# Kernel tuning notes

Hardware: AMD Instinct MI355X
Metric: run time of the kernel (lower is better)

The kernel has to match this reference:

```python
import jax, jax.numpy as jnp
import numpy as np

B, N, C, H, T = 64, 4096, 768, 12, 10


def setup_inputs() -> dict:
    key = jax.random.key(0)
    kx, kq, kk, kv, kp = jax.random.split(key, 5)
    std = 0.02  # trunc_normal std from _init_weights
    return {
        "x": jax.random.normal(kx, (B, N, C), jnp.float32),
        "Wq": std * jax.random.normal(kq, (C, C), jnp.float32),
        "Wk": std * jax.random.normal(kk, (C, C), jnp.float32),
        "Wv": std * jax.random.normal(kv, (C, C), jnp.float32),
        "Wp": std * jax.random.normal(kp, (C, C), jnp.float32),
        "bp": jnp.zeros((C,), jnp.float32),
        "nb_task_tokens": T,
    }


def reference(x, Wq, Wk, Wv, Wp, bp, nb_task_tokens):
    Bq, Nq, Cq = x.shape
    d = Cq // H
    scale = d ** -0.5
    Tt = nb_task_tokens
    # q only from the first T (task) tokens; k, v from all N tokens
    q = (x[:, :Tt] @ Wq).reshape(Bq, Tt, H, d).transpose(0, 2, 1, 3) * scale  # [B,H,T,d]
    k = (x @ Wk).reshape(Bq, Nq, H, d).transpose(0, 2, 1, 3)                  # [B,H,N,d]
    v = (x @ Wv).reshape(Bq, Nq, H, d).transpose(0, 2, 1, 3)                  # [B,H,N,d]
    attn = jnp.einsum("bhtd,bhnd->bhtn", q, k)                                # [B,H,T,N]
    # mask: task token i may attend to itself and to all patch tokens (cols >= T),
    # but not to other task tokens
    rows = jnp.arange(Tt)[:, None]
    cols = jnp.arange(Nq)[None, :]
    allowed = (cols >= Tt) | (cols == rows)                                   # [T,N]
    attn = jnp.where(allowed, attn, -jnp.inf)
    attn = jax.nn.softmax(attn, axis=-1)
    x_cls = jnp.einsum("bhtn,bhnd->bhtd", attn, v)                            # [B,H,T,d]
    x_cls = x_cls.transpose(0, 2, 1, 3).reshape(Bq, Tt, Cq)
    x_cls = x_cls @ Wp + bp
    return (x_cls, attn, v)
```

## Files before the change

### kernel.cpp

```cpp
#include <hip/hip_runtime.h>

typedef __attribute__((ext_vector_type(8))) short short8;
typedef __attribute__((ext_vector_type(4))) short short4v;
typedef __attribute__((ext_vector_type(4))) float f32x4;

__device__ __forceinline__ unsigned short f2bf(float f) {
  union { float f; unsigned u; } v; v.f = f;
  unsigned r = v.u + 0x7FFFu + ((v.u >> 16) & 1u);
  return (unsigned short)(r >> 16);
}

__device__ __forceinline__ void gload16(const void* g, void* l) {
  __builtin_amdgcn_global_load_lds(
      (const __attribute__((address_space(1))) void*)g,
      (__attribute__((address_space(3))) void*)l, 16, 0, 0);
}

__global__ __launch_bounds__(256) void conv_x(const float* __restrict__ x,
                                              unsigned short* __restrict__ xb) {
  const long total = 25165824;
  long stride = (long)gridDim.x * 256;
  for (long u = blockIdx.x * 256 + threadIdx.x; u < total; u += stride) {
    const float* p = x + u * 8;
    float4 a = *(const float4*)p;
    float4 b = *(const float4*)(p + 4);
    short8 h;
    h[0] = (short)f2bf(a.x); h[1] = (short)f2bf(a.y);
    h[2] = (short)f2bf(a.z); h[3] = (short)f2bf(a.w);
    h[4] = (short)f2bf(b.x); h[5] = (short)f2bf(b.y);
    h[6] = (short)f2bf(b.z); h[7] = (short)f2bf(b.w);
    *(short8*)(xb + u * 8) = h;
  }
}

__global__ __launch_bounds__(256) void prep_w(const float* __restrict__ Wk,
                                              const float* __restrict__ Wv,
                                              unsigned short* __restrict__ Wt) {
  int idx = blockIdx.x * 256 + threadIdx.x;
  int n = idx / 768, k = idx - n * 768;
  float w = (n < 768) ? Wk[k * 768 + n] : Wv[k * 768 + (n - 768)];
  Wt[idx] = f2bf(w);
}

__global__ __launch_bounds__(256) void q_proj(const float* __restrict__ x,
                                              const float* __restrict__ Wq,
                                              unsigned short* __restrict__ q_ws) {
  int b = blockIdx.x, tid = threadIdx.x;
  __shared__ float xr[7680];
  const float* xp = x + (long)b * 4096 * 768;
  for (int i = tid; i < 7680; i += 256) xr[i] = xp[i];
  for (int i = tid; i < 12 * 6 * 64; i += 256) {
    int h = i / 384, rem = i - h * 384;
    int t = 10 + rem / 64, d = rem & 63;
    q_ws[(((long)(b * 12 + h) * 16 + t) << 6) + d] = 0;
  }
  __syncthreads();
  float acc[10][3];
#pragma unroll
  for (int t = 0; t < 10; ++t) { acc[t][0] = 0.f; acc[t][1] = 0.f; acc[t][2] = 0.f; }
  for (int k = 0; k < 768; ++k) {
    const float* wr = Wq + (long)k * 768;
    float w0 = wr[tid], w1 = wr[tid + 256], w2 = wr[tid + 512];
#pragma unroll
    for (int t = 0; t < 10; ++t) {
      float xv = xr[t * 768 + k];
      acc[t][0] += xv * w0; acc[t][1] += xv * w1; acc[t][2] += xv * w2;
    }
  }
#pragma unroll
  for (int t = 0; t < 10; ++t) {
#pragma unroll
    for (int j = 0; j < 3; ++j) {
      int c = tid + j * 256;
      int h = c >> 6, d = c & 63;
      q_ws[(((long)(b * 12 + h) * 16 + t) << 6) + d] = f2bf(acc[t][j] * 0.125f);
    }
  }
}

__global__ __launch_bounds__(512, 2) void gemm_kv8(const unsigned short* __restrict__ xb,
                                                   const unsigned short* __restrict__ Wt,
                                                   unsigned short* __restrict__ k_ws,
                                                   float* __restrict__ v_out) {
  __shared__ char smem[131072];
#define A0T ((unsigned short*)(smem))
#define B0T ((unsigned short*)(smem + 32768))
#define A1T ((unsigned short*)(smem + 65536))
#define B1T ((unsigned short*)(smem + 98304))

  int bid = blockIdx.x;
  int lb = (bid & 7) * 768 + (bid >> 3);
  int mt = lb / 6, nt = lb - mt * 6;
  long m0 = (long)mt * 256; int n0 = nt * 256;
  int tid = threadIdx.x, lane = tid & 63;
  int uw = __builtin_amdgcn_readfirstlane(tid >> 6);
  int wm = uw >> 2, wn = uw & 3;
  int r16 = lane & 15, gk = lane >> 4;

  const unsigned short* xs = xb + m0 * 768;
  const unsigned short* wp = Wt + (long)n0 * 768;

  int srow8 = lane >> 3;
  int sch = ((lane & 7) ^ (srow8 & 7)) << 3;
  const unsigned short* sA = xs + (long)(uw * 8 + srow8) * 768 + sch;
  const unsigned short* sB = wp + (long)(uw * 8 + srow8) * 768 + sch;

  int ck0 = ((gk ^ (r16 & 7)) << 3);
  int ck1 = (((4 + gk) ^ (r16 & 7)) << 3);
  int arb = (wm * 128 + r16) * 64;
  int brb = (wn * 64 + r16) * 64;

  f32x4 acc[8][4];
#pragma unroll
  for (int i = 0; i < 8; ++i)
#pragma unroll
    for (int j = 0; j < 4; ++j) acc[i][j] = (f32x4){0.f, 0.f, 0.f, 0.f};

#define SGA(AT, I, KO) gload16(sA + (long)(I) * 49152 + (KO), (AT) + ((I) * 64 + uw * 8) * 64)
#define SGB(BT, I, KO) gload16(sB + (long)(I) * 49152 + (KO), (BT) + ((I) * 64 + uw * 8) * 64)
#define WBND asm volatile("s_waitcnt vmcnt(0)\n\ts_barrier" ::: "memory")
#define PBAR __builtin_amdgcn_s_barrier()

#define BODY(AC, BC, AN, BN, KOS, DOST)                                         \
  {                                                                             \
    short8 fa[4][2], fb0[2][2], fb1[2][2];                                      \
                    \
    if (DOST) { SGA(AN, 0, KOS); SGA(AN, 1, KOS); SGB(BN, 0, KOS); SGB(BN, 1, KOS); } \
    _Pragma("unroll")                                                           \
    for (int mi = 0; mi < 4; ++mi) {                                            \
      fa[mi][0] = *(const short8*)&AC[arb + mi * 1024 + ck0];                   \
      fa[mi][1] = *(const short8*)&AC[arb + mi * 1024 + ck1];                   \
    }                                                                           \
    _Pragma("unroll")                                                           \
    for (int ni = 0; ni < 2; ++ni) {                                            \
      fb0[ni][0] = *(const short8*)&BC[brb + ni * 1024 + ck0];                  \
      fb0[ni][1] = *(const short8*)&BC[brb + ni * 1024 + ck1];                  \
    }                                                                           \
    PBAR;                                                                       \
    __builtin_amdgcn_s_setprio(1);                                              \
    _Pragma("unroll")                                                           \
    for (int mi = 0; mi < 4; ++mi)                                              \
      _Pragma("unroll")                                                         \
      for (int ni = 0; ni < 2; ++ni) {                                          \
        acc[mi][ni] = __builtin_amdgcn_mfma_f32_16x16x32_bf16(fa[mi][0], fb0[ni][0], acc[mi][ni], 0, 0, 0); \
        acc[mi][ni] = __builtin_amdgcn_mfma_f32_16x16x32_bf16(fa[mi][1], fb0[ni][1], acc[mi][ni], 0, 0, 0); \
      }                                                                         \
    __builtin_amdgcn_s_setprio(0);                                              \
    PBAR;                                                                       \
                           \
    if (DOST) { SGA(AN, 2, KOS); SGA(AN, 3, KOS); SGB(BN, 2, KOS); SGB(BN, 3, KOS); } \
    _Pragma("unroll")                                                           \
    for (int ni = 0; ni < 2; ++ni) {                                            \
      fb1[ni][0] = *(const short8*)&BC[brb + (ni + 2) * 1024 + ck0];            \
      fb1[ni][1] = *(const short8*)&BC[brb + (ni + 2) * 1024 + ck1];            \
    }                                                                           \
    PBAR;                                                                       \
    __builtin_amdgcn_s_setprio(1);                                              \
    _Pragma("unroll")                                                           \
    for (int mi = 0; mi < 4; ++mi)                                              \
      _Pragma("unroll")                                                         \
      for (int ni = 0; ni < 2; ++ni) {                                          \
        acc[mi][ni + 2] = __builtin_amdgcn_mfma_f32_16x16x32_bf16(fa[mi][0], fb1[ni][0], acc[mi][ni + 2], 0, 0, 0); \
        acc[mi][ni + 2] = __builtin_amdgcn_mfma_f32_16x16x32_bf16(fa[mi][1], fb1[ni][1], acc[mi][ni + 2], 0, 0, 0); \
      }                                                                         \
    __builtin_amdgcn_s_setprio(0);                                              \
    PBAR;                                                                       \
                                       \
    _Pragma("unroll")                                                           \
    for (int mi = 0; mi < 4; ++mi) {                                            \
      fa[mi][0] = *(const short8*)&AC[arb + (mi + 4) * 1024 + ck0];             \
      fa[mi][1] = *(const short8*)&AC[arb + (mi + 4) * 1024 + ck1];             \
    }                                                                           \
    PBAR;                                                                       \
    __builtin_amdgcn_s_setprio(1);                                              \
    _Pragma("unroll")                                                           \
    for (int mi = 0; mi < 4; ++mi)                                              \
      _Pragma("unroll")                                                         \
      for (int ni = 0; ni < 2; ++ni) {                                          \
        acc[mi + 4][ni + 2] = __builtin_amdgcn_mfma_f32_16x16x32_bf16(fa[mi][0], fb1[ni][0], acc[mi + 4][ni + 2], 0, 0, 0); \
        acc[mi + 4][ni + 2] = __builtin_amdgcn_mfma_f32_16x16x32_bf16(fa[mi][1], fb1[ni][1], acc[mi + 4][ni + 2], 0, 0, 0); \
      }                                                                         \
    __builtin_amdgcn_s_setprio(0);                                              \
    PBAR;                                                                       \
                                 \
    __builtin_amdgcn_s_setprio(1);                                              \
    _Pragma("unroll")                                                           \
    for (int mi = 0; mi < 4; ++mi)                                              \
      _Pragma("unroll")                                                         \
      for (int ni = 0; ni < 2; ++ni) {                                          \
        acc[mi + 4][ni] = __builtin_amdgcn_mfma_f32_16x16x32_bf16(fa[mi][0], fb0[ni][0], acc[mi + 4][ni], 0, 0, 0); \
        acc[mi + 4][ni] = __builtin_amdgcn_mfma_f32_16x16x32_bf16(fa[mi][1], fb0[ni][1], acc[mi + 4][ni], 0, 0, 0); \
      }                                                                         \
    __builtin_amdgcn_s_setprio(0);                                              \
  }

  SGA(A0T, 0, 0); SGA(A0T, 1, 0); SGA(A0T, 2, 0); SGA(A0T, 3, 0);
  SGB(B0T, 0, 0); SGB(B0T, 1, 0); SGB(B0T, 2, 0); SGB(B0T, 3, 0);
  WBND;

#pragma unroll 1
  for (int t = 0; t < 12; t += 2) {
    BODY(A0T, B0T, A1T, B1T, (t + 1) * 64, true);
    WBND;
    BODY(A1T, B1T, A0T, B0T, (t + 2) * 64, (t + 2) < 12);
    WBND;
  }
#undef BODY
#undef SGA
#undef SGB
#undef WBND
#undef PBAR

  float* scr = (float*)smem + uw * 1088;
  bool is_k = (n0 < 768);
  int h = (is_k ? (n0 >> 6) : ((n0 - 768) >> 6)) + wn;
  int bq = (int)(m0 >> 12);
  int nb = (int)(m0 & 4095) + wm * 128;

#pragma unroll
  for (int mi = 0; mi < 8; ++mi) {
#pragma unroll
    for (int ni = 0; ni < 4; ++ni)
#pragma unroll
      for (int r = 0; r < 4; ++r)
        scr[(gk * 4 + r) * 68 + ni * 16 + r16] = acc[mi][ni][r];
    int nbase = nb + mi * 16;
    if (is_k) {
#pragma unroll
      for (int p = 0; p < 2; ++p) {
        int row = p * 8 + (lane >> 3), d0 = (lane & 7) << 3;
        float4 aa = *(const float4*)&scr[row * 68 + d0];
        float4 bb = *(const float4*)&scr[row * 68 + d0 + 4];
        short8 hh;
        hh[0] = (short)f2bf(aa.x); hh[1] = (short)f2bf(aa.y);
        hh[2] = (short)f2bf(aa.z); hh[3] = (short)f2bf(aa.w);
        hh[4] = (short)f2bf(bb.x); hh[5] = (short)f2bf(bb.y);
        hh[6] = (short)f2bf(bb.z); hh[7] = (short)f2bf(bb.w);
        *(short8*)&k_ws[((long)(bq * 12 + h) * 4096 + nbase + row) * 64 + d0] = hh;
      }
    } else {
#pragma unroll
      for (int p = 0; p < 4; ++p) {
        int row = p * 4 + (lane >> 4), d0 = (lane & 15) << 2;
        float4 aa = *(const float4*)&scr[row * 68 + d0];
        *(float4*)&v_out[((long)(bq * 12 + h) * 4096 + nbase + row) * 64 + d0] = aa;
      }
    }
  }
#undef A0T
#undef B0T
#undef A1T
#undef B1T
}

__global__ __launch_bounds__(256) void gemm_kv(const float* __restrict__ x,
                                               const unsigned short* __restrict__ Wt,
                                               unsigned short* __restrict__ k_ws,
                                               float* __restrict__ v_out) {
  __shared__ char lds[32768];
  int bid = blockIdx.x;
  int lb = (bid & 7) * 3072 + (bid >> 3);
  int mt = lb / 12, nt = lb - mt * 12;
  long m0 = (long)mt * 128; int n0 = nt * 128;
  int tid = threadIdx.x, lane = tid & 63;
  int wid = tid >> 6, wm = wid >> 1, wn = wid & 1;
  int rlo = lane & 15, gk = lane >> 4;

  const float* xs = x + m0 * 768;
  const unsigned short* wp = Wt + (long)n0 * 768;

  int arow0 = tid >> 3, ak4 = (tid & 7) << 2;
  int bn = tid >> 1, bg = (tid & 1) << 1;

  f32x4 acc[4][4];
#pragma unroll
  for (int i = 0; i < 4; ++i)
#pragma unroll
    for (int j = 0; j < 4; ++j) acc[i][j] = (f32x4){0.f, 0.f, 0.f, 0.f};

  float4 fA[4]; short8 wB[2];
#pragma unroll
  for (int it = 0; it < 4; ++it) {
    int row = it * 32 + arow0;
    fA[it] = *(const float4*)(xs + (long)row * 768 + ak4);
  }
#pragma unroll
  for (int i = 0; i < 2; ++i)
    wB[i] = *(const short8*)(wp + (long)bn * 768 + (bg + i) * 8);
#pragma unroll
  for (int it = 0; it < 4; ++it) {
    int row = it * 32 + arow0;
    short4v h;
    h[0] = (short)f2bf(fA[it].x); h[1] = (short)f2bf(fA[it].y);
    h[2] = (short)f2bf(fA[it].z); h[3] = (short)f2bf(fA[it].w);
    *(short4v*)(lds + row * 64 + ((ak4 * 2) ^ (((row >> 1) & 3) << 4))) = h;
  }
#pragma unroll
  for (int i = 0; i < 2; ++i)
    *(short8*)(lds + 16384 + bn * 64 + (((bg + i) * 16) ^ (((bn >> 1) & 3) << 4))) = wB[i];
  __syncthreads();

#pragma unroll 2
  for (int ks = 0; ks < 24; ++ks) {
    char* Ab = lds + (ks & 1) * 8192;
    char* Bb = lds + 16384 + (ks & 1) * 8192;
    bool pf = (ks + 1 < 24);
    if (pf) {
#pragma unroll
      for (int it = 0; it < 4; ++it) {
        int row = it * 32 + arow0;
        fA[it] = *(const float4*)(xs + (long)row * 768 + (ks + 1) * 32 + ak4);
      }
#pragma unroll
      for (int i = 0; i < 2; ++i)
        wB[i] = *(const short8*)(wp + (long)bn * 768 + (ks + 1) * 32 + (bg + i) * 8);
    }
    short8 af[4], bfr[4];
#pragma unroll
    for (int mi = 0; mi < 4; ++mi) {
      int row = wm * 64 + mi * 16 + rlo;
      af[mi] = *(const short8*)(Ab + row * 64 + ((gk * 16) ^ (((row >> 1) & 3) << 4)));
    }
#pragma unroll
    for (int ni = 0; ni < 4; ++ni) {
      int n = wn * 64 + ni * 16 + rlo;
      bfr[ni] = *(const short8*)(Bb + n * 64 + ((gk * 16) ^ (((n >> 1) & 3) << 4)));
    }
#pragma unroll
    for (int mi = 0; mi < 4; ++mi)
#pragma unroll
      for (int ni = 0; ni < 4; ++ni)
        acc[mi][ni] = __builtin_amdgcn_mfma_f32_16x16x32_bf16(af[mi], bfr[ni], acc[mi][ni], 0, 0, 0);
    if (pf) {
      char* An = lds + ((ks + 1) & 1) * 8192;
      char* Bn = lds + 16384 + ((ks + 1) & 1) * 8192;
#pragma unroll
      for (int it = 0; it < 4; ++it) {
        int row = it * 32 + arow0;
        short4v h;
        h[0] = (short)f2bf(fA[it].x); h[1] = (short)f2bf(fA[it].y);
        h[2] = (short)f2bf(fA[it].z); h[3] = (short)f2bf(fA[it].w);
        *(short4v*)(An + row * 64 + ((ak4 * 2) ^ (((row >> 1) & 3) << 4))) = h;
      }
#pragma unroll
      for (int i = 0; i < 2; ++i)
        *(short8*)(Bn + bn * 64 + (((bg + i) * 16) ^ (((bn >> 1) & 3) << 4))) = wB[i];
    }
    __syncthreads();
  }

  bool is_k = (n0 < 768);
  int cb = is_k ? n0 : n0 - 768;
#pragma unroll
  for (int ni = 0; ni < 4; ++ni) {
    int cc = cb + wn * 64 + ni * 16 + rlo;
    int h = cc >> 6, d = cc & 63;
#pragma unroll
    for (int mi = 0; mi < 4; ++mi) {
#pragma unroll
      for (int r = 0; r < 4; ++r) {
        long m = m0 + wm * 64 + mi * 16 + gk * 4 + r;
        int b = (int)(m >> 12), n = (int)(m & 4095);
        long off = ((long)(b * 12 + h) * 4096 + n) * 64 + d;
        float val = acc[mi][ni][r];
        if (is_k) k_ws[off] = f2bf(val);
        else      v_out[off] = val;
      }
    }
  }
}

__global__ __launch_bounds__(512) void attn_fused(const unsigned short* __restrict__ k_ws,
                                                  const unsigned short* __restrict__ q_ws,
                                                  const float* __restrict__ v_glob,
                                                  float* __restrict__ attn_out,
                                                  float* __restrict__ preproj) {
  __shared__ float red[8][16];
  __shared__ float rowmax[16];
  __shared__ float rowinv[16];
  __shared__ float scratch[8 * 256];

  int tid = threadIdx.x, lane = tid & 63, w = tid >> 6;
  int bh = blockIdx.x;
  int r16 = lane & 15, gk = lane >> 4;
  int trc = (r16 < 10) ? r16 : 9;

  const unsigned short* kp = k_ws + (long)bh * (4096 * 64);
  const unsigned short* qp = q_ws + (long)bh * 1024;
  float* sraw = attn_out + (long)bh * 40960;
  const float* vp = v_glob + (long)bh * (4096 * 64);

  short8 qf0 = *(const short8*)(qp + r16 * 64 + gk * 8);
  short8 qf1 = *(const short8*)(qp + r16 * 64 + 32 + gk * 8);

  float pmax = -3.0e38f;
  for (int ch = 0; ch < 32; ++ch) {
    int n0 = (w * 32 + ch) << 4;
    short8 kf0 = *(const short8*)(kp + (long)(n0 + r16) * 64 + gk * 8);
    short8 kf1 = *(const short8*)(kp + (long)(n0 + r16) * 64 + 32 + gk * 8);
    f32x4 d4 = (f32x4){0.f, 0.f, 0.f, 0.f};
    d4 = __builtin_amdgcn_mfma_f32_16x16x32_bf16(kf0, qf0, d4, 0, 0, 0);
    d4 = __builtin_amdgcn_mfma_f32_16x16x32_bf16(kf1, qf1, d4, 0, 0, 0);
    float sv[4];
#pragma unroll
    for (int r = 0; r < 4; ++r) {
      int n = n0 + gk * 4 + r;
      float s = d4[r];
      if (n < 10 && n != r16) s = -1e30f;
      sv[r] = s;
      pmax = fmaxf(pmax, s);
    }
    if (r16 < 10)
      *(float4*)(sraw + r16 * 4096 + n0 + gk * 4) = make_float4(sv[0], sv[1], sv[2], sv[3]);
  }
  pmax = fmaxf(pmax, __shfl_xor(pmax, 16));
  pmax = fmaxf(pmax, __shfl_xor(pmax, 32));
  if (lane < 16) red[w][lane] = pmax;
  __syncthreads();
  if (tid < 16) {
    float m = red[0][tid];
#pragma unroll
    for (int i = 1; i < 8; ++i) m = fmaxf(m, red[i][tid]);
    rowmax[tid] = m;
  }
  __syncthreads();

  float mx = rowmax[trc];
  float psum = 0.f;
  for (int ch = 0; ch < 16; ++ch) {
    int n0 = ((w * 16 + ch) << 5) + gk * 8;
    float4 a = *(const float4*)(sraw + trc * 4096 + n0);
    float4 b2 = *(const float4*)(sraw + trc * 4096 + n0 + 4);
    psum += __expf(a.x - mx) + __expf(a.y - mx) + __expf(a.z - mx) + __expf(a.w - mx)
          + __expf(b2.x - mx) + __expf(b2.y - mx) + __expf(b2.z - mx) + __expf(b2.w - mx);
  }
  psum += __shfl_xor(psum, 16);
  psum += __shfl_xor(psum, 32);
  if (lane < 16) red[w][lane] = psum;
  __syncthreads();
  if (tid < 16) {
    float s = 0.f;
#pragma unroll
    for (int i = 0; i < 8; ++i) s += red[i][tid];
    rowinv[tid] = 1.0f / s;
  }
  __syncthreads();

  int dc = w & 3, half = w >> 2;
  int d0 = dc << 4;
  float inv = rowinv[trc];
  f32x4 acc = (f32x4){0.f, 0.f, 0.f, 0.f};
  for (int kk = 0; kk < 64; ++kk) {
    int nr = half * 2048 + kk * 32 + gk * 8;
    float* sp = sraw + trc * 4096 + nr;
    float4 s0 = *(const float4*)(sp);
    float4 s1 = *(const float4*)(sp + 4);
    float p0 = __expf(s0.x - mx) * inv, p1 = __expf(s0.y - mx) * inv;
    float p2 = __expf(s0.z - mx) * inv, p3 = __expf(s0.w - mx) * inv;
    float p4 = __expf(s1.x - mx) * inv, p5 = __expf(s1.y - mx) * inv;
    float p6 = __expf(s1.z - mx) * inv, p7 = __expf(s1.w - mx) * inv;
    if (r16 < 10) {
      *(float4*)(sp)     = make_float4(p0, p1, p2, p3);
      *(float4*)(sp + 4) = make_float4(p4, p5, p6, p7);
    }
    short8 pa;
    pa[0] = (short)f2bf(p0); pa[1] = (short)f2bf(p1);
    pa[2] = (short)f2bf(p2); pa[3] = (short)f2bf(p3);
    pa[4] = (short)f2bf(p4); pa[5] = (short)f2bf(p5);
    pa[6] = (short)f2bf(p6); pa[7] = (short)f2bf(p7);
    short8 vb;
    const float* vrow = vp + (long)nr * 64 + d0 + r16;
#pragma unroll
    for (int j = 0; j < 8; ++j) vb[j] = (short)f2bf(vrow[j * 64]);
    acc = __builtin_amdgcn_mfma_f32_16x16x32_bf16(pa, vb, acc, 0, 0, 0);
  }
#pragma unroll
  for (int r = 0; r < 4; ++r)
    scratch[w * 256 + (gk * 4 + r) * 16 + r16] = acc[r];
  __syncthreads();

  int b = bh / 12, h = bh - b * 12;
  for (int idx = tid; idx < 640; idx += 512) {
    int tt = idx >> 6, d = idx & 63;
    int c = d >> 4, dl = d & 15;
    float s = scratch[c * 256 + tt * 16 + dl] + scratch[(c + 4) * 256 + tt * 16 + dl];
    preproj[((long)b * 10 + tt) * 768 + h * 64 + d] = s;
  }
}

__global__ __launch_bounds__(256) void proj_out_k(const float* __restrict__ preproj,
                                                  const float* __restrict__ Wp,
                                                  const float* __restrict__ bp,
                                                  float* __restrict__ out0) {
  int b = blockIdx.x, tid = threadIdx.x;
  __shared__ float xr[7680];
  const float* pp = preproj + (long)b * 7680;
  for (int i = tid; i < 7680; i += 256) xr[i] = pp[i];
  __syncthreads();
  float acc[10][3];
#pragma unroll
  for (int t = 0; t < 10; ++t) { acc[t][0] = 0.f; acc[t][1] = 0.f; acc[t][2] = 0.f; }
  for (int k = 0; k < 768; ++k) {
    const float* wr = Wp + (long)k * 768;
    float w0 = wr[tid], w1 = wr[tid + 256], w2 = wr[tid + 512];
#pragma unroll
    for (int t = 0; t < 10; ++t) {
      float xv = xr[t * 768 + k];
      acc[t][0] += xv * w0; acc[t][1] += xv * w1; acc[t][2] += xv * w2;
    }
  }
  float b0 = bp[tid], b1 = bp[tid + 256], b2 = bp[tid + 512];
  float* op = out0 + (long)b * 7680;
#pragma unroll
  for (int t = 0; t < 10; ++t) {
    op[t * 768 + tid]       = acc[t][0] + b0;
    op[t * 768 + tid + 256] = acc[t][1] + b1;
    op[t * 768 + tid + 512] = acc[t][2] + b2;
  }
}

extern "C" void kernel_launch(void* const* d_in, const int* in_sizes, int n_in,
                              void* d_out, int out_size, void* d_ws, size_t ws_size,
                              hipStream_t stream) {
  (void)in_sizes; (void)n_in; (void)out_size;
  const float* x  = (const float*)d_in[0];
  const float* Wq = (const float*)d_in[1];
  const float* Wk = (const float*)d_in[2];
  const float* Wv = (const float*)d_in[3];
  const float* Wp = (const float*)d_in[4];
  const float* bp = (const float*)d_in[5];

  float* out      = (float*)d_out;
  float* attn_out = out + 491520;
  float* v_out    = out + 31948800;

  char* ws = (char*)d_ws;
  const size_t NEED_BIG = 811204608;

  if (ws_size >= NEED_BIG) {
    unsigned short* x_bf16 = (unsigned short*)(ws);
    unsigned short* k_ws = (unsigned short*)(ws + 402653184);
    unsigned short* q_ws = (unsigned short*)(ws + 805306368);
    unsigned short* Wt   = (unsigned short*)(ws + 806879232);
    float* preproj       = (float*)(ws + 809238528);

    conv_x<<<dim3(2048), dim3(256), 0, stream>>>(x, x_bf16);
    prep_w<<<dim3(4608), dim3(256), 0, stream>>>(Wk, Wv, Wt);
    q_proj<<<dim3(64), dim3(256), 0, stream>>>(x, Wq, q_ws);
    gemm_kv8<<<dim3(6144), dim3(512), 0, stream>>>(x_bf16, Wt, k_ws, v_out);
    attn_fused<<<dim3(768), dim3(512), 0, stream>>>(k_ws, q_ws, v_out, attn_out, preproj);
    proj_out_k<<<dim3(64), dim3(256), 0, stream>>>(preproj, Wp, bp, out);
  } else {
    unsigned short* k_ws = (unsigned short*)(ws);
    unsigned short* q_ws = (unsigned short*)(ws + 402653184);
    unsigned short* Wt   = (unsigned short*)(ws + 404226048);
    float* preproj       = (float*)(ws + 406585344);

    prep_w<<<dim3(4608), dim3(256), 0, stream>>>(Wk, Wv, Wt);
    q_proj<<<dim3(64), dim3(256), 0, stream>>>(x, Wq, q_ws);
    gemm_kv<<<dim3(24576), dim3(256), 0, stream>>>(x, Wt, k_ws, v_out);
    attn_fused<<<dim3(768), dim3(512), 0, stream>>>(k_ws, q_ws, v_out, attn_out, preproj);
    proj_out_k<<<dim3(64), dim3(256), 0, stream>>>(preproj, Wp, bp, out);
  }
}
```

Before: 1.606 ms.

## Keep attention scores in registers and compute PV per-wave over own key range

The attention kernel now holds all 32 score tiles per wave in registers instead of writing raw scores to the global attn buffer and re-reading them twice. It computes exp once, writes normalized probabilities once, and stages bf16 probabilities in swizzled LDS. Each wave then does the PV product over its own 512-key range for all four d-chunks, with an 8-way partial reduction in LDS. This removes two passes over the global attn rows and redundant exp work, in exchange for higher register pressure (128 floats of scores per thread) and a larger LDS footprint that may limit occupancy.

```diff
diff --git a/kernel.cpp b/kernel.cpp
--- a/kernel.cpp
+++ b/kernel.cpp
@@ -124,7 +124,6 @@
 #define BODY(AC, BC, AN, BN, KOS, DOST)                                         \
   {                                                                             \
     short8 fa[4][2], fb0[2][2], fb1[2][2];                                      \
-                    \
     if (DOST) { SGA(AN, 0, KOS); SGA(AN, 1, KOS); SGB(BN, 0, KOS); SGB(BN, 1, KOS); } \
     _Pragma("unroll")                                                           \
     for (int mi = 0; mi < 4; ++mi) {                                            \
@@ -147,7 +146,6 @@
       }                                                                         \
     __builtin_amdgcn_s_setprio(0);                                              \
     PBAR;                                                                       \
-                           \
     if (DOST) { SGA(AN, 2, KOS); SGA(AN, 3, KOS); SGB(BN, 2, KOS); SGB(BN, 3, KOS); } \
     _Pragma("unroll")                                                           \
     for (int ni = 0; ni < 2; ++ni) {                                            \
@@ -165,7 +163,6 @@
       }                                                                         \
     __builtin_amdgcn_s_setprio(0);                                              \
     PBAR;                                                                       \
-                                       \
     _Pragma("unroll")                                                           \
     for (int mi = 0; mi < 4; ++mi) {                                            \
       fa[mi][0] = *(const short8*)&AC[arb + (mi + 4) * 1024 + ck0];             \
@@ -182,7 +179,6 @@
       }                                                                         \
     __builtin_amdgcn_s_setprio(0);                                              \
     PBAR;                                                                       \
-                                 \
     __builtin_amdgcn_s_setprio(1);                                              \
     _Pragma("unroll")                                                           \
     for (int mi = 0; mi < 4; ++mi)                                              \
@@ -370,20 +366,22 @@
   }
 }
 
-__global__ __launch_bounds__(512) void attn_fused(const unsigned short* __restrict__ k_ws,
-                                                  const unsigned short* __restrict__ q_ws,
-                                                  const float* __restrict__ v_glob,
-                                                  float* __restrict__ attn_out,
-                                                  float* __restrict__ preproj) {
-  __shared__ float red[8][16];
-  __shared__ float rowmax[16];
-  __shared__ float rowinv[16];
-  __shared__ float scratch[8 * 256];
+__global__ __launch_bounds__(512) void attn_fused2(const unsigned short* __restrict__ k_ws,
+                                                   const unsigned short* __restrict__ q_ws,
+                                                   const float* __restrict__ v_glob,
+                                                   float* __restrict__ attn_out,
+                                                   float* __restrict__ preproj) {
+  __shared__ char blob[81920 + 32768 + 1024];
+  unsigned short* pbuf = (unsigned short*)blob;
+  float* part = (float*)(blob + 81920);
+  float* redm = (float*)(blob + 114688);
+  float* rowmax16 = redm + 128;
+  float* rowinv16 = rowmax16 + 16;
 
   int tid = threadIdx.x, lane = tid & 63, w = tid >> 6;
   int bh = blockIdx.x;
   int r16 = lane & 15, gk = lane >> 4;
-  int trc = (r16 < 10) ? r16 : 9;
+  int nW = w << 9;
 
   const unsigned short* kp = k_ws + (long)bh * (4096 * 64);
   const unsigned short* qp = q_ws + (long)bh * 1024;
@@ -393,98 +391,109 @@
   short8 qf0 = *(const short8*)(qp + r16 * 64 + gk * 8);
   short8 qf1 = *(const short8*)(qp + r16 * 64 + 32 + gk * 8);
 
+  f32x4 s[32];
   float pmax = -3.0e38f;
+#pragma unroll
   for (int ch = 0; ch < 32; ++ch) {
-    int n0 = (w * 32 + ch) << 4;
+    int n0 = nW + (ch << 4);
     short8 kf0 = *(const short8*)(kp + (long)(n0 + r16) * 64 + gk * 8);
     short8 kf1 = *(const short8*)(kp + (long)(n0 + r16) * 64 + 32 + gk * 8);
     f32x4 d4 = (f32x4){0.f, 0.f, 0.f, 0.f};
     d4 = __builtin_amdgcn_mfma_f32_16x16x32_bf16(kf0, qf0, d4, 0, 0, 0);
     d4 = __builtin_amdgcn_mfma_f32_16x16x32_bf16(kf1, qf1, d4, 0, 0, 0);
-    float sv[4];
 #pragma unroll
     for (int r = 0; r < 4; ++r) {
       int n = n0 + gk * 4 + r;
-      float s = d4[r];
-      if (n < 10 && n != r16) s = -1e30f;
-      sv[r] = s;
-      pmax = fmaxf(pmax, s);
-    }
-    if (r16 < 10)
-      *(float4*)(sraw + r16 * 4096 + n0 + gk * 4) = make_float4(sv[0], sv[1], sv[2], sv[3]);
+      float v = d4[r];
+      if (n < 10 && n != r16) v = -1e30f;
+      d4[r] = v;
+      pmax = fmaxf(pmax, v);
+    }
+    s[ch] = d4;
   }
   pmax = fmaxf(pmax, __shfl_xor(pmax, 16));
   pmax = fmaxf(pmax, __shfl_xor(pmax, 32));
-  if (lane < 16) red[w][lane] = pmax;
+  if (lane < 16) redm[w * 16 + lane] = pmax;
   __syncthreads();
   if (tid < 16) {
-    float m = red[0][tid];
-#pragma unroll
-    for (int i = 1; i < 8; ++i) m = fmaxf(m, red[i][tid]);
-    rowmax[tid] = m;
-  }
-  __syncthreads();
-
-  float mx = rowmax[trc];
+    float m = redm[tid];
+#pragma unroll
+    for (int i = 1; i < 8; ++i) m = fmaxf(m, redm[i * 16 + tid]);
+    rowmax16[tid] = m;
+  }
+  __syncthreads();
+  float mx = rowmax16[r16];
+
   float psum = 0.f;
-  for (int ch = 0; ch < 16; ++ch) {
-    int n0 = ((w * 16 + ch) << 5) + gk * 8;
-    float4 a = *(const float4*)(sraw + trc * 4096 + n0);
-    float4 b2 = *(const float4*)(sraw + trc * 4096 + n0 + 4);
-    psum += __expf(a.x - mx) + __expf(a.y - mx) + __expf(a.z - mx) + __expf(a.w - mx)
-          + __expf(b2.x - mx) + __expf(b2.y - mx) + __expf(b2.z - mx) + __expf(b2.w - mx);
+#pragma unroll
+  for (int ch = 0; ch < 32; ++ch) {
+    f32x4 e;
+#pragma unroll
+    for (int r = 0; r < 4; ++r) {
+      e[r] = __expf(s[ch][r] - mx);
+      psum += e[r];
+    }
+    s[ch] = e;
   }
   psum += __shfl_xor(psum, 16);
   psum += __shfl_xor(psum, 32);
-  if (lane < 16) red[w][lane] = psum;
+  if (lane < 16) redm[w * 16 + lane] = psum;
   __syncthreads();
   if (tid < 16) {
-    float s = 0.f;
-#pragma unroll
-    for (int i = 0; i < 8; ++i) s += red[i][tid];
-    rowinv[tid] = 1.0f / s;
-  }
-  __syncthreads();
-
-  int dc = w & 3, half = w >> 2;
-  int d0 = dc << 4;
-  float inv = rowinv[trc];
-  f32x4 acc = (f32x4){0.f, 0.f, 0.f, 0.f};
-  for (int kk = 0; kk < 64; ++kk) {
-    int nr = half * 2048 + kk * 32 + gk * 8;
-    float* sp = sraw + trc * 4096 + nr;
-    float4 s0 = *(const float4*)(sp);
-    float4 s1 = *(const float4*)(sp + 4);
-    float p0 = __expf(s0.x - mx) * inv, p1 = __expf(s0.y - mx) * inv;
-    float p2 = __expf(s0.z - mx) * inv, p3 = __expf(s0.w - mx) * inv;
-    float p4 = __expf(s1.x - mx) * inv, p5 = __expf(s1.y - mx) * inv;
-    float p6 = __expf(s1.z - mx) * inv, p7 = __expf(s1.w - mx) * inv;
+    float t = 0.f;
+#pragma unroll
+    for (int i = 0; i < 8; ++i) t += redm[i * 16 + tid];
+    rowinv16[tid] = 1.0f / t;
+  }
+  __syncthreads();
+  float inv = rowinv16[r16];
+
+  char* pb = (char*)pbuf + w * 10240 + r16 * 1024;
+  int swz = (r16 & 7) << 4;
+#pragma unroll
+  for (int ch = 0; ch < 32; ++ch) {
+    float p0 = s[ch][0] * inv, p1 = s[ch][1] * inv;
+    float p2 = s[ch][2] * inv, p3 = s[ch][3] * inv;
     if (r16 < 10) {
-      *(float4*)(sp)     = make_float4(p0, p1, p2, p3);
-      *(float4*)(sp + 4) = make_float4(p4, p5, p6, p7);
-    }
-    short8 pa;
-    pa[0] = (short)f2bf(p0); pa[1] = (short)f2bf(p1);
-    pa[2] = (short)f2bf(p2); pa[3] = (short)f2bf(p3);
-    pa[4] = (short)f2bf(p4); pa[5] = (short)f2bf(p5);
-    pa[6] = (short)f2bf(p6); pa[7] = (short)f2bf(p7);
-    short8 vb;
-    const float* vrow = vp + (long)nr * 64 + d0 + r16;
-#pragma unroll
-    for (int j = 0; j < 8; ++j) vb[j] = (short)f2bf(vrow[j * 64]);
-    acc = __builtin_amdgcn_mfma_f32_16x16x32_bf16(pa, vb, acc, 0, 0, 0);
-  }
-#pragma unroll
-  for (int r = 0; r < 4; ++r)
-    scratch[w * 256 + (gk * 4 + r) * 16 + r16] = acc[r];
+      *(float4*)(sraw + r16 * 4096 + nW + (ch << 4) + gk * 4) = make_float4(p0, p1, p2, p3);
+      short4v h4;
+      h4[0] = (short)f2bf(p0); h4[1] = (short)f2bf(p1);
+      h4[2] = (short)f2bf(p2); h4[3] = (short)f2bf(p3);
+      *(short4v*)(pb + ((((ch << 4) + gk * 4) * 2) ^ swz)) = h4;
+    }
+  }
+
+  f32x4 pacc[4];
+#pragma unroll
+  for (int dc = 0; dc < 4; ++dc) pacc[dc] = (f32x4){0.f, 0.f, 0.f, 0.f};
+#pragma unroll 2
+  for (int ks = 0; ks < 16; ++ks) {
+    short8 pa = *(const short8*)(pb + (((ks * 32 + gk * 8) * 2) ^ swz));
+    const float* vbase = vp + (long)(nW + ks * 32 + gk * 8) * 64 + r16;
+#pragma unroll
+    for (int dc = 0; dc < 4; ++dc) {
+      short8 vb;
+      const float* vrow = vbase + dc * 16;
+#pragma unroll
+      for (int j = 0; j < 8; ++j) vb[j] = (short)f2bf(vrow[j * 64]);
+      pacc[dc] = __builtin_amdgcn_mfma_f32_16x16x32_bf16(pa, vb, pacc[dc], 0, 0, 0);
+    }
+  }
+#pragma unroll
+  for (int dc = 0; dc < 4; ++dc)
+#pragma unroll
+    for (int r = 0; r < 4; ++r)
+      part[w * 1024 + dc * 256 + (gk * 4 + r) * 16 + r16] = pacc[dc][r];
   __syncthreads();
 
   int b = bh / 12, h = bh - b * 12;
   for (int idx = tid; idx < 640; idx += 512) {
     int tt = idx >> 6, d = idx & 63;
-    int c = d >> 4, dl = d & 15;
-    float s = scratch[c * 256 + tt * 16 + dl] + scratch[(c + 4) * 256 + tt * 16 + dl];
-    preproj[((long)b * 10 + tt) * 768 + h * 64 + d] = s;
+    int dc = d >> 4, dl = d & 15;
+    float sum = 0.f;
+#pragma unroll
+    for (int i = 0; i < 8; ++i) sum += part[i * 1024 + dc * 256 + tt * 16 + dl];
+    preproj[((long)b * 10 + tt) * 768 + h * 64 + d] = sum;
   }
 }
 
@@ -548,7 +557,7 @@
     prep_w<<<dim3(4608), dim3(256), 0, stream>>>(Wk, Wv, Wt);
     q_proj<<<dim3(64), dim3(256), 0, stream>>>(x, Wq, q_ws);
     gemm_kv8<<<dim3(6144), dim3(512), 0, stream>>>(x_bf16, Wt, k_ws, v_out);
-    attn_fused<<<dim3(768), dim3(512), 0, stream>>>(k_ws, q_ws, v_out, attn_out, preproj);
+    attn_fused2<<<dim3(768), dim3(512), 0, stream>>>(k_ws, q_ws, v_out, attn_out, preproj);
     proj_out_k<<<dim3(64), dim3(256), 0, stream>>>(preproj, Wp, bp, out);
   } else {
     unsigned short* k_ws = (unsigned short*)(ws);
@@ -559,7 +568,7 @@
     prep_w<<<dim3(4608), dim3(256), 0, stream>>>(Wk, Wv, Wt);
     q_proj<<<dim3(64), dim3(256), 0, stream>>>(x, Wq, q_ws);
     gemm_kv<<<dim3(24576), dim3(256), 0, stream>>>(x, Wt, k_ws, v_out);
-    attn_fused<<<dim3(768), dim3(512), 0, stream>>>(k_ws, q_ws, v_out, attn_out, preproj);
+    attn_fused2<<<dim3(768), dim3(512), 0, stream>>>(k_ws, q_ws, v_out, attn_out, preproj);
     proj_out_k<<<dim3(64), dim3(256), 0, stream>>>(preproj, Wp, bp, out);
   }
 }
```

After: 1.495 ms. 1.07x faster.
